# Kernel optimization log

Hardware: AMD Instinct MI355X
Metric: run time of the kernel (lower is better)

Reference implementation:

```python
import jax, jax.numpy as jnp
import numpy as np
from jax import lax

N = 100000        # nodes
E = 3200000       # edges (avg degree 32)
F_IN = 128        # num_features
DIM = 16          # conv1 out
HID = 16          # conv2 out


def _gcn_layer(x, W, b, row, col, n):
    """PyG GCNConv: h = x @ W; add self-loops; symmetric deg^-1/2 norm;
    aggregate messages from source (row) at target (col); add bias."""
    h = x @ W                                   # [n, out]
    loop = jnp.arange(n)
    r = jnp.concatenate([row, loop])            # sources incl. self-loops
    c = jnp.concatenate([col, loop])            # targets incl. self-loops
    deg = jax.ops.segment_sum(jnp.ones(r.shape[0], dtype=h.dtype), c, num_segments=n)
    dinv = jnp.where(deg > 0, lax.rsqrt(deg), jnp.zeros((), h.dtype))
    norm = dinv[r] * dinv[c]                    # [E+n]
    out = jax.ops.segment_sum(h[r] * norm[:, None], c, num_segments=n)
    return out + b


def setup_inputs() -> dict:
    key = jax.random.key(0)
    k1, k2, k3, k4, k5, k6 = jax.random.split(key, 6)
    x = jax.random.normal(k1, (N, F_IN), dtype=jnp.float32)
    edge_index = jax.random.randint(k2, (2, E), 0, N, dtype=jnp.int64)
    # GCNConv weights (glorot-ish scale) and zero-init biases (PyG default init style)
    W1 = jax.random.normal(k3, (F_IN, DIM), dtype=jnp.float32) * (1.0 / np.sqrt(F_IN))
    b1 = jnp.zeros((DIM,), dtype=jnp.float32)
    W2 = jax.random.normal(k4, (DIM, HID), dtype=jnp.float32) * (1.0 / np.sqrt(DIM))
    b2 = jnp.zeros((HID,), dtype=jnp.float32)
    return {"x": x, "edge_index": edge_index, "W1": W1, "b1": b1, "W2": W2, "b2": b2}


def reference(x, edge_index, W1, b1, W2, b2):
    row, col = edge_index[0], edge_index[1]
    h = jax.nn.relu(_gcn_layer(x, W1, b1, row, col, N))
    out = jax.nn.relu(_gcn_layer(h, W2, b2, row, col, N))
    return out
```

## Files before the change

kernel.cpp:

```cpp
#include <hip/hip_runtime.h>
#include <hip/hip_fp16.h>

#define N_NODES 100000
#define N_EDGES 3200000
#define F_IN    128
#define DIM     16

#define SUP_SH  9
#define NSUP    196
#define SCAP    17920
#define CHA     4096
#define NBLKA   ((N_EDGES + CHA - 1) / CHA)
#define NCAP    96

static inline size_t alignup(size_t x) { return (x + 255) & ~(size_t)255; }

__global__ void zero_init(int* __restrict__ cursorA) {
    cursorA[threadIdx.x] = 0;
}

__global__ __launch_bounds__(512) void partA(const int* __restrict__ row,
                                             const int* __restrict__ col,
                                             int* __restrict__ cursorA,
                                             unsigned* __restrict__ stageA) {
    __shared__ int hist[256], lstart[256], lcur[256], gbase[256], scanT[256];
    __shared__ unsigned stg[CHA];
    __shared__ unsigned char stgb[CHA];
    const int t = threadIdx.x;
    const int e0 = blockIdx.x * CHA;
    const int nv = min(CHA, N_EDGES - e0);
    const int i0 = t * 8;
    const bool act = (i0 < nv);

    if (t < 256) hist[t] = 0;

    int4 c0, c1, r0, r1;
    if (act) {
        c0 = *(const int4*)(col + e0 + i0);
        c1 = *(const int4*)(col + e0 + i0 + 4);
        r0 = *(const int4*)(row + e0 + i0);
        r1 = *(const int4*)(row + e0 + i0 + 4);
    }
    __syncthreads();
    if (act) {
        atomicAdd(&hist[(unsigned)c0.x >> SUP_SH], 1);
        atomicAdd(&hist[(unsigned)c0.y >> SUP_SH], 1);
        atomicAdd(&hist[(unsigned)c0.z >> SUP_SH], 1);
        atomicAdd(&hist[(unsigned)c0.w >> SUP_SH], 1);
        atomicAdd(&hist[(unsigned)c1.x >> SUP_SH], 1);
        atomicAdd(&hist[(unsigned)c1.y >> SUP_SH], 1);
        atomicAdd(&hist[(unsigned)c1.z >> SUP_SH], 1);
        atomicAdd(&hist[(unsigned)c1.w >> SUP_SH], 1);
    }
    __syncthreads();
    int v = 0;
    if (t < 256) { v = hist[t]; scanT[t] = v; }
    __syncthreads();
#pragma unroll
    for (int off = 1; off < 256; off <<= 1) {
        int a = (t >= off && t < 256) ? scanT[t - off] : 0;
        __syncthreads();
        if (t < 256) scanT[t] += a;
        __syncthreads();
    }
    if (t < 256) {
        int ex = scanT[t] - v;
        lstart[t] = ex; lcur[t] = ex;
        if (v) {
            int gb = atomicAdd(&cursorA[t], v);
            if (gb + v > SCAP) gb = SCAP - v;
            gbase[t] = t * SCAP + gb;
        }
    }
    __syncthreads();
    if (act) {
        int cc[8] = { c0.x, c0.y, c0.z, c0.w, c1.x, c1.y, c1.z, c1.w };
        int rr[8] = { r0.x, r0.y, r0.z, r0.w, r1.x, r1.y, r1.z, r1.w };
#pragma unroll
        for (int q = 0; q < 8; ++q) {
            int sp = (unsigned)cc[q] >> SUP_SH;
            int p = atomicAdd(&lcur[sp], 1);
            stg[p] = (unsigned)rr[q] | ((unsigned)(cc[q] & 511) << 17);
            stgb[p] = (unsigned char)sp;
        }
    }
    __syncthreads();
    for (int i = t; i < nv; i += 512) {
        int sp = stgb[i];
        stageA[gbase[sp] + (i - lstart[sp])] = stg[i];
    }
}

__global__ __launch_bounds__(1024) void partB(const unsigned* __restrict__ stageA,
                                              const int* __restrict__ cursorA,
                                              int* __restrict__ nodeCur,
                                              unsigned* __restrict__ csr) {
    __shared__ int lcur[512];
    const int t = threadIdx.x;
    const int sup = blockIdx.x;
    const int nbase = sup << SUP_SH;
    if (t < 512) lcur[t] = (nbase + t) * NCAP;
    __syncthreads();
    const int base = sup * SCAP;
    const int cnt = min(cursorA[sup], SCAP);
    for (int i = t; i < cnt; i += 1024) {
        unsigned v = stageA[base + i];
        int n = (v >> 17) & 511;
        int pos = atomicAdd(&lcur[n], 1);
        if (pos < (nbase + n) * NCAP + NCAP)
            csr[pos] = (v & 0x1FFFFu) << 3;
    }
    __syncthreads();
    if (t < 512) {
        int node = nbase + t;
        if (node < N_NODES) nodeCur[node] = min(lcur[t] - node * NCAP, NCAP);
    }
}

__global__ __launch_bounds__(256) void gemm1(const float* __restrict__ x,
                                             const float* __restrict__ W,
                                             const int* __restrict__ nodeCur,
                                             __half* __restrict__ hd) {
    __shared__ float4 sW4[F_IN * DIM / 4];
    __shared__ float4 sX4[16][F_IN / 4 + 1];
    const int t = threadIdx.x;
#pragma unroll
    for (int i = t; i < F_IN * DIM / 4; i += 256) sW4[i] = ((const float4*)W)[i];
    const int base = blockIdx.x * 16;
#pragma unroll
    for (int i = t; i < 16 * (F_IN / 4); i += 256) {
        int r = i >> 5, k4 = i & 31;
        sX4[r][k4] = ((const float4*)(x + (size_t)(base + r) * F_IN))[k4];
    }
    __syncthreads();
    const float* sW = (const float*)sW4;
    const int rrow = t >> 4, cj = t & 15;
    const float* xr = (const float*)&sX4[rrow][0];
    float acc = 0.f;
#pragma unroll
    for (int k = 0; k < F_IN; ++k) acc += xr[k] * sW[k * DIM + cj];
    const float dc = rsqrtf((float)nodeCur[base + rrow] + 1.0f);
    hd[(size_t)(base + rrow) * DIM + cj] = __float2half(acc * dc);
}

__device__ __forceinline__ void node_gather(const unsigned* __restrict__ csr,
                                            const __half2* __restrict__ h2,
                                            int p, int end, int f,
                                            float& ax, float& ay) {
    for (; p + 15 < end; p += 16) {
        uint4 ea = *(const uint4*)(csr + p);
        uint4 eb = *(const uint4*)(csr + p + 4);
        uint4 ec = *(const uint4*)(csr + p + 8);
        uint4 ed = *(const uint4*)(csr + p + 12);
        float2 v0 = __half22float2(h2[ea.x + f]);
        float2 v1 = __half22float2(h2[ea.y + f]);
        float2 v2 = __half22float2(h2[ea.z + f]);
        float2 v3 = __half22float2(h2[ea.w + f]);
        float2 v4 = __half22float2(h2[eb.x + f]);
        float2 v5 = __half22float2(h2[eb.y + f]);
        float2 v6 = __half22float2(h2[eb.z + f]);
        float2 v7 = __half22float2(h2[eb.w + f]);
        float2 v8 = __half22float2(h2[ec.x + f]);
        float2 v9 = __half22float2(h2[ec.y + f]);
        float2 va = __half22float2(h2[ec.z + f]);
        float2 vb = __half22float2(h2[ec.w + f]);
        float2 vc = __half22float2(h2[ed.x + f]);
        float2 vd = __half22float2(h2[ed.y + f]);
        float2 ve = __half22float2(h2[ed.z + f]);
        float2 vf = __half22float2(h2[ed.w + f]);
        ax += (((v0.x + v1.x) + (v2.x + v3.x)) + ((v4.x + v5.x) + (v6.x + v7.x)))
            + (((v8.x + v9.x) + (va.x + vb.x)) + ((vc.x + vd.x) + (ve.x + vf.x)));
        ay += (((v0.y + v1.y) + (v2.y + v3.y)) + ((v4.y + v5.y) + (v6.y + v7.y)))
            + (((v8.y + v9.y) + (va.y + vb.y)) + ((vc.y + vd.y) + (ve.y + vf.y)));
    }
    if (p + 7 < end) {
        uint4 ea = *(const uint4*)(csr + p);
        uint4 eb = *(const uint4*)(csr + p + 4);
        float2 v0 = __half22float2(h2[ea.x + f]);
        float2 v1 = __half22float2(h2[ea.y + f]);
        float2 v2 = __half22float2(h2[ea.z + f]);
        float2 v3 = __half22float2(h2[ea.w + f]);
        float2 v4 = __half22float2(h2[eb.x + f]);
        float2 v5 = __half22float2(h2[eb.y + f]);
        float2 v6 = __half22float2(h2[eb.z + f]);
        float2 v7 = __half22float2(h2[eb.w + f]);
        ax += ((v0.x + v1.x) + (v2.x + v3.x)) + ((v4.x + v5.x) + (v6.x + v7.x));
        ay += ((v0.y + v1.y) + (v2.y + v3.y)) + ((v4.y + v5.y) + (v6.y + v7.y));
        p += 8;
    }
    if (p + 3 < end) {
        uint4 e4 = *(const uint4*)(csr + p);
        float2 v0 = __half22float2(h2[e4.x + f]);
        float2 v1 = __half22float2(h2[e4.y + f]);
        float2 v2 = __half22float2(h2[e4.z + f]);
        float2 v3 = __half22float2(h2[e4.w + f]);
        ax += (v0.x + v1.x) + (v2.x + v3.x);
        ay += (v0.y + v1.y) + (v2.y + v3.y);
        p += 4;
    }
    for (; p < end; ++p) {
        float2 v = __half22float2(h2[csr[p] + f]);
        ax += v.x; ay += v.y;
    }
}

__global__ __launch_bounds__(256) void agg1(const unsigned* __restrict__ csr,
                                            const int* __restrict__ nodeCur,
                                            const __half2* __restrict__ hd,
                                            const float* __restrict__ b1,
                                            const float* __restrict__ W2,
                                            __half2* __restrict__ hd2) {
    __shared__ float sW2[DIM * DIM];
    __shared__ float sb1[DIM];
    const int t = threadIdx.x;
    sW2[t] = W2[t];
    if (t < DIM) sb1[t] = b1[t];
    __syncthreads();
    const int lane = t & 63, f = lane & 7;
    const int node = blockIdx.x * 32 + ((t >> 6) << 3) + (lane >> 3);
    const int degv = nodeCur[node];
    const float dc = rsqrtf((float)degv + 1.0f);
    const int p0 = node * NCAP;
    float ax = 0.f, ay = 0.f;
    node_gather(csr, hd, p0, p0 + degv, f, ax, ay);
    float2 sv = __half22float2(hd[(size_t)node * 8 + f]);
    float fx = dc * (ax + sv.x) + sb1[2 * f];
    float fy = dc * (ay + sv.y) + sb1[2 * f + 1];
    fx = fmaxf(fx, 0.f); fy = fmaxf(fy, 0.f);
    float sx = 0.f, sy = 0.f;
    const int gl = lane & 56;
#pragma unroll
    for (int mq = 0; mq < 8; ++mq) {
        float lo = __shfl(fx, gl + mq, 64);
        float hi = __shfl(fy, gl + mq, 64);
        sx += lo * sW2[(2 * mq) * DIM + 2 * f]     + hi * sW2[(2 * mq + 1) * DIM + 2 * f];
        sy += lo * sW2[(2 * mq) * DIM + 2 * f + 1] + hi * sW2[(2 * mq + 1) * DIM + 2 * f + 1];
    }
    hd2[(size_t)node * 8 + f] = __floats2half2_rn(dc * sx, dc * sy);
}

__global__ __launch_bounds__(256) void agg2(const unsigned* __restrict__ csr,
                                            const int* __restrict__ nodeCur,
                                            const __half2* __restrict__ hd2,
                                            const float* __restrict__ b2,
                                            float2* __restrict__ out2) {
    __shared__ float sb2[DIM];
    const int t = threadIdx.x;
    if (t < DIM) sb2[t] = b2[t];
    __syncthreads();
    const int lane = t & 63, f = lane & 7;
    const int node = blockIdx.x * 32 + ((t >> 6) << 3) + (lane >> 3);
    const int degv = nodeCur[node];
    const float dc = rsqrtf((float)degv + 1.0f);
    const int p0 = node * NCAP;
    float ax = 0.f, ay = 0.f;
    node_gather(csr, hd2, p0, p0 + degv, f, ax, ay);
    float2 sv = __half22float2(hd2[(size_t)node * 8 + f]);
    float fx = dc * (ax + sv.x) + sb2[2 * f];
    float fy = dc * (ay + sv.y) + sb2[2 * f + 1];
    out2[(size_t)node * 8 + f] = make_float2(fmaxf(fx, 0.f), fmaxf(fy, 0.f));
}

extern "C" void kernel_launch(void* const* d_in, const int* in_sizes, int n_in,
                              void* d_out, int out_size, void* d_ws, size_t ws_size,
                              hipStream_t stream) {
    const float* x   = (const float*)d_in[0];
    const int*   ei  = (const int*)d_in[1];
    const float* W1  = (const float*)d_in[2];
    const float* b1  = (const float*)d_in[3];
    const float* W2  = (const float*)d_in[4];
    const float* b2  = (const float*)d_in[5];
    float*       out = (float*)d_out;

    const int* row = ei;
    const int* col = ei + N_EDGES;

    char* ws = (char*)d_ws;
    size_t o = 0;
    auto take = [&](size_t bytes) { char* p = ws + o; o = alignup(o + bytes); return p; };
    int*      nodeCur = (int*)     take((size_t)N_NODES * 4);
    int*      cursorA = (int*)     take((size_t)256 * 4);
    unsigned* stageA  = (unsigned*)take((size_t)NSUP * SCAP * 4);
    unsigned* csr     = (unsigned*)take((size_t)N_NODES * NCAP * 4);

    __half* hd  = (__half*)stageA;
    __half* hd2 = (__half*)((char*)stageA + alignup((size_t)N_NODES * DIM * 2));

    zero_init<<<1, 256, 0, stream>>>(cursorA);
    partA<<<NBLKA, 512, 0, stream>>>(row, col, cursorA, stageA);
    partB<<<NSUP, 1024, 0, stream>>>(stageA, cursorA, nodeCur, csr);

    gemm1<<<N_NODES / 16, 256, 0, stream>>>(x, W1, nodeCur, hd);
    agg1<<<N_NODES / 32, 256, 0, stream>>>(csr, nodeCur, (const __half2*)hd,
                                           b1, W2, (__half2*)hd2);
    agg2<<<N_NODES / 32, 256, 0, stream>>>(csr, nodeCur, (const __half2*)hd2,
                                           b2, (float2*)out);
}
```

Measured before the change: 128.1 us.

## Fuse feature GEMM into edge partition kernel and apply degree scaling in partB

The x@W1 GEMM now runs as extra blocks in the same launch as the edge-partition pass, so the bandwidth-bound GEMM overlaps the partitioning work. The degree normalization moves into partB, which rescales the unscaled half-precision features once node degrees are known. This drops the separate gemm1 launch and its serial dependency on partB. In exchange it adds an extra half-precision round trip over the features and needs separate workspace buffers instead of reusing the staging area.

```diff
diff --git a/kernel.cpp b/kernel.cpp
--- a/kernel.cpp
+++ b/kernel.cpp
@@ -12,6 +12,8 @@
 #define CHA     4096
 #define NBLKA   ((N_EDGES + CHA - 1) / CHA)
 #define NCAP    96
+#define GROWS   32
+#define NBLKG   (N_NODES / GROWS)
 
 static inline size_t alignup(size_t x) { return (x + 255) & ~(size_t)255; }
 
@@ -19,83 +21,117 @@
     cursorA[threadIdx.x] = 0;
 }
 
-__global__ __launch_bounds__(512) void partA(const int* __restrict__ row,
-                                             const int* __restrict__ col,
-                                             int* __restrict__ cursorA,
-                                             unsigned* __restrict__ stageA) {
-    __shared__ int hist[256], lstart[256], lcur[256], gbase[256], scanT[256];
-    __shared__ unsigned stg[CHA];
-    __shared__ unsigned char stgb[CHA];
+__global__ __launch_bounds__(512) void partA_gemm(const int* __restrict__ row,
+                                                  const int* __restrict__ col,
+                                                  int* __restrict__ cursorA,
+                                                  unsigned* __restrict__ stageA,
+                                                  const float* __restrict__ x,
+                                                  const float* __restrict__ W,
+                                                  __half* __restrict__ hu) {
+    __shared__ __align__(16) char smem[25600];
     const int t = threadIdx.x;
-    const int e0 = blockIdx.x * CHA;
-    const int nv = min(CHA, N_EDGES - e0);
-    const int i0 = t * 8;
-    const bool act = (i0 < nv);
-
-    if (t < 256) hist[t] = 0;
-
-    int4 c0, c1, r0, r1;
-    if (act) {
-        c0 = *(const int4*)(col + e0 + i0);
-        c1 = *(const int4*)(col + e0 + i0 + 4);
-        r0 = *(const int4*)(row + e0 + i0);
-        r1 = *(const int4*)(row + e0 + i0 + 4);
-    }
-    __syncthreads();
-    if (act) {
-        atomicAdd(&hist[(unsigned)c0.x >> SUP_SH], 1);
-        atomicAdd(&hist[(unsigned)c0.y >> SUP_SH], 1);
-        atomicAdd(&hist[(unsigned)c0.z >> SUP_SH], 1);
-        atomicAdd(&hist[(unsigned)c0.w >> SUP_SH], 1);
-        atomicAdd(&hist[(unsigned)c1.x >> SUP_SH], 1);
-        atomicAdd(&hist[(unsigned)c1.y >> SUP_SH], 1);
-        atomicAdd(&hist[(unsigned)c1.z >> SUP_SH], 1);
-        atomicAdd(&hist[(unsigned)c1.w >> SUP_SH], 1);
-    }
-    __syncthreads();
-    int v = 0;
-    if (t < 256) { v = hist[t]; scanT[t] = v; }
-    __syncthreads();
-#pragma unroll
-    for (int off = 1; off < 256; off <<= 1) {
-        int a = (t >= off && t < 256) ? scanT[t - off] : 0;
-        __syncthreads();
-        if (t < 256) scanT[t] += a;
-        __syncthreads();
-    }
-    if (t < 256) {
-        int ex = scanT[t] - v;
-        lstart[t] = ex; lcur[t] = ex;
-        if (v) {
-            int gb = atomicAdd(&cursorA[t], v);
-            if (gb + v > SCAP) gb = SCAP - v;
-            gbase[t] = t * SCAP + gb;
-        }
-    }
-    __syncthreads();
-    if (act) {
-        int cc[8] = { c0.x, c0.y, c0.z, c0.w, c1.x, c1.y, c1.z, c1.w };
-        int rr[8] = { r0.x, r0.y, r0.z, r0.w, r1.x, r1.y, r1.z, r1.w };
-#pragma unroll
-        for (int q = 0; q < 8; ++q) {
-            int sp = (unsigned)cc[q] >> SUP_SH;
-            int p = atomicAdd(&lcur[sp], 1);
-            stg[p] = (unsigned)rr[q] | ((unsigned)(cc[q] & 511) << 17);
-            stgb[p] = (unsigned char)sp;
-        }
-    }
-    __syncthreads();
-    for (int i = t; i < nv; i += 512) {
-        int sp = stgb[i];
-        stageA[gbase[sp] + (i - lstart[sp])] = stg[i];
+
+    if (blockIdx.x < NBLKA) {
+        int* hist   = (int*)smem;
+        int* lstart = hist + 256;
+        int* lcur   = hist + 512;
+        int* gbase  = hist + 768;
+        int* scanT  = hist + 1024;
+        unsigned* stg = (unsigned*)(smem + 5120);
+        unsigned char* stgb = (unsigned char*)(smem + 21504);
+
+        const int e0 = blockIdx.x * CHA;
+        const int nv = min(CHA, N_EDGES - e0);
+        const int i0 = t * 8;
+        const bool act = (i0 < nv);
+
+        if (t < 256) hist[t] = 0;
+
+        int4 c0, c1, r0, r1;
+        if (act) {
+            c0 = *(const int4*)(col + e0 + i0);
+            c1 = *(const int4*)(col + e0 + i0 + 4);
+            r0 = *(const int4*)(row + e0 + i0);
+            r1 = *(const int4*)(row + e0 + i0 + 4);
+        }
+        __syncthreads();
+        if (act) {
+            atomicAdd(&hist[(unsigned)c0.x >> SUP_SH], 1);
+            atomicAdd(&hist[(unsigned)c0.y >> SUP_SH], 1);
+            atomicAdd(&hist[(unsigned)c0.z >> SUP_SH], 1);
+            atomicAdd(&hist[(unsigned)c0.w >> SUP_SH], 1);
+            atomicAdd(&hist[(unsigned)c1.x >> SUP_SH], 1);
+            atomicAdd(&hist[(unsigned)c1.y >> SUP_SH], 1);
+            atomicAdd(&hist[(unsigned)c1.z >> SUP_SH], 1);
+            atomicAdd(&hist[(unsigned)c1.w >> SUP_SH], 1);
+        }
+        __syncthreads();
+        int v = 0;
+        if (t < 256) { v = hist[t]; scanT[t] = v; }
+        __syncthreads();
+#pragma unroll
+        for (int off = 1; off < 256; off <<= 1) {
+            int a = (t >= off && t < 256) ? scanT[t - off] : 0;
+            __syncthreads();
+            if (t < 256) scanT[t] += a;
+            __syncthreads();
+        }
+        if (t < 256) {
+            int ex = scanT[t] - v;
+            lstart[t] = ex; lcur[t] = ex;
+            if (v) {
+                int gb = atomicAdd(&cursorA[t], v);
+                if (gb + v > SCAP) gb = SCAP - v;
+                gbase[t] = t * SCAP + gb;
+            }
+        }
+        __syncthreads();
+        if (act) {
+            int cc[8] = { c0.x, c0.y, c0.z, c0.w, c1.x, c1.y, c1.z, c1.w };
+            int rr[8] = { r0.x, r0.y, r0.z, r0.w, r1.x, r1.y, r1.z, r1.w };
+#pragma unroll
+            for (int q = 0; q < 8; ++q) {
+                int sp = (unsigned)cc[q] >> SUP_SH;
+                int p = atomicAdd(&lcur[sp], 1);
+                stg[p] = (unsigned)rr[q] | ((unsigned)(cc[q] & 511) << 17);
+                stgb[p] = (unsigned char)sp;
+            }
+        }
+        __syncthreads();
+        for (int i = t; i < nv; i += 512) {
+            int sp = stgb[i];
+            stageA[gbase[sp] + (i - lstart[sp])] = stg[i];
+        }
+    } else {
+        float4* sW4 = (float4*)smem;
+        float4 (*sX4)[F_IN / 4 + 1] = (float4 (*)[F_IN / 4 + 1])(smem + 8192);
+        const int gb = blockIdx.x - NBLKA;
+        const int base = gb * GROWS;
+        sW4[t] = ((const float4*)W)[t];
+#pragma unroll
+        for (int i = t; i < GROWS * (F_IN / 4); i += 512) {
+            int r = i >> 5, k4 = i & 31;
+            sX4[r][k4] = ((const float4*)(x + (size_t)(base + r) * F_IN))[k4];
+        }
+        __syncthreads();
+        const float* sW = (const float*)sW4;
+        const int rrow = t >> 4, cj = t & 15;
+        const float* xr = (const float*)&sX4[rrow][0];
+        float acc = 0.f;
+#pragma unroll
+        for (int k = 0; k < F_IN; ++k) acc += xr[k] * sW[k * DIM + cj];
+        hu[(size_t)(base + rrow) * DIM + cj] = __float2half(acc);
     }
 }
 
 __global__ __launch_bounds__(1024) void partB(const unsigned* __restrict__ stageA,
                                               const int* __restrict__ cursorA,
                                               int* __restrict__ nodeCur,
-                                              unsigned* __restrict__ csr) {
+                                              unsigned* __restrict__ csr,
+                                              const __half2* __restrict__ hu,
+                                              __half2* __restrict__ hd) {
     __shared__ int lcur[512];
+    __shared__ float dl[512];
     const int t = threadIdx.x;
     const int sup = blockIdx.x;
     const int nbase = sup << SUP_SH;
@@ -113,34 +149,20 @@
     __syncthreads();
     if (t < 512) {
         int node = nbase + t;
-        if (node < N_NODES) nodeCur[node] = min(lcur[t] - node * NCAP, NCAP);
-    }
-}
-
-__global__ __launch_bounds__(256) void gemm1(const float* __restrict__ x,
-                                             const float* __restrict__ W,
-                                             const int* __restrict__ nodeCur,
-                                             __half* __restrict__ hd) {
-    __shared__ float4 sW4[F_IN * DIM / 4];
-    __shared__ float4 sX4[16][F_IN / 4 + 1];
-    const int t = threadIdx.x;
-#pragma unroll
-    for (int i = t; i < F_IN * DIM / 4; i += 256) sW4[i] = ((const float4*)W)[i];
-    const int base = blockIdx.x * 16;
-#pragma unroll
-    for (int i = t; i < 16 * (F_IN / 4); i += 256) {
-        int r = i >> 5, k4 = i & 31;
-        sX4[r][k4] = ((const float4*)(x + (size_t)(base + r) * F_IN))[k4];
-    }
-    __syncthreads();
-    const float* sW = (const float*)sW4;
-    const int rrow = t >> 4, cj = t & 15;
-    const float* xr = (const float*)&sX4[rrow][0];
-    float acc = 0.f;
-#pragma unroll
-    for (int k = 0; k < F_IN; ++k) acc += xr[k] * sW[k * DIM + cj];
-    const float dc = rsqrtf((float)nodeCur[base + rrow] + 1.0f);
-    hd[(size_t)(base + rrow) * DIM + cj] = __float2half(acc * dc);
+        if (node < N_NODES) {
+            int deg = min(lcur[t] - node * NCAP, NCAP);
+            nodeCur[node] = deg;
+            dl[t] = rsqrtf((float)deg + 1.0f);
+        }
+    }
+    __syncthreads();
+    const int nn = min(N_NODES - nbase, 512);
+    for (int idx = t; idx < nn * 8; idx += 1024) {
+        int nl = idx >> 3, f = idx & 7;
+        float2 vf = __half22float2(hu[(size_t)(nbase + nl) * 8 + f]);
+        float d = dl[nl];
+        hd[(size_t)(nbase + nl) * 8 + f] = __floats2half2_rn(vf.x * d, vf.y * d);
+    }
 }
 
 __device__ __forceinline__ void node_gather(const unsigned* __restrict__ csr,
@@ -282,15 +304,16 @@
     int*      cursorA = (int*)     take((size_t)256 * 4);
     unsigned* stageA  = (unsigned*)take((size_t)NSUP * SCAP * 4);
     unsigned* csr     = (unsigned*)take((size_t)N_NODES * NCAP * 4);
-
-    __half* hd  = (__half*)stageA;
-    __half* hd2 = (__half*)((char*)stageA + alignup((size_t)N_NODES * DIM * 2));
+    __half*   hu      = (__half*)  take((size_t)N_NODES * DIM * 2);
+    __half*   hd      = (__half*)  take((size_t)N_NODES * DIM * 2);
+    __half*   hd2     = (__half*)  take((size_t)N_NODES * DIM * 2);
 
     zero_init<<<1, 256, 0, stream>>>(cursorA);
-    partA<<<NBLKA, 512, 0, stream>>>(row, col, cursorA, stageA);
-    partB<<<NSUP, 1024, 0, stream>>>(stageA, cursorA, nodeCur, csr);
-
-    gemm1<<<N_NODES / 16, 256, 0, stream>>>(x, W1, nodeCur, hd);
+    partA_gemm<<<NBLKA + NBLKG, 512, 0, stream>>>(row, col, cursorA, stageA,
+                                                  x, W1, hu);
+    partB<<<NSUP, 1024, 0, stream>>>(stageA, cursorA, nodeCur, csr,
+                                     (const __half2*)hu, (__half2*)hd);
+
     agg1<<<N_NODES / 32, 256, 0, stream>>>(csr, nodeCur, (const __half2*)hd,
                                            b1, W2, (__half2*)hd2);
     agg2<<<N_NODES / 32, 256, 0, stream>>>(csr, nodeCur, (const __half2*)hd2,
```

Result: faster. 121.4 us (-5.2%).
